# Performance work log

Hardware: AMD Instinct MI355X
Metric: run time of the kernel (lower is better)

Reference implementation:

```python
import jax, jax.numpy as jnp
import numpy as np

K_BINS, EMB_WIDTH = 2048, 64
N, T = 8, 8192

def setup_inputs() -> dict:
    key = jax.random.key(0)
    k1, k2 = jax.random.split(key)
    x = jax.random.normal(k1, (N, EMB_WIDTH, T), dtype=jnp.float32)
    mask = jnp.ones((N, 1, T), dtype=jnp.float32)
    k = jax.random.normal(k2, (K_BINS, EMB_WIDTH), dtype=jnp.float32)
    return {"x": x, "mask": mask, "k": k}

def reference(x, mask, k):
    # Faithful forward of BottleneckBlock.forward with update_k=False and
    # codebook `k` already initialized (init path is a stateful randperm init).
    n, c, t = x.shape
    w = k.shape[1]
    # preprocess: [N, W, T] -> [N*T, W]
    xf = jnp.transpose(x, (0, 2, 1)).reshape(-1, c)
    mf = jnp.transpose(mask, (0, 2, 1)).reshape(-1, 1)
    prenorm = jnp.linalg.norm(xf - jnp.mean(xf)) / np.sqrt(float(xf.size))
    dist = (jnp.sum(xf * xf, axis=-1, keepdims=True)
            - 2.0 * (xf @ k.T)
            + jnp.sum(k * k, axis=-1)[None, :])  # [N*T, k_bins]
    x_l = jnp.argmin(dist, axis=-1)              # [N*T]
    fit = jax.lax.stop_gradient(jnp.mean(jnp.min(dist, axis=-1)))
    x_d = jax.lax.stop_gradient(k[x_l])          # dequantize, no_grad in torch
    # commit loss: mask is 0/1, so masked-row norm^2 == sum(mask * diff^2)
    diff2 = jnp.sum((x_d - xf) ** 2, axis=-1, keepdims=True)
    commit_loss = jnp.sum(mf * diff2) / (jnp.sum(mf) * w)
    # straight-through estimator + mask
    x_d = (xf + jax.lax.stop_gradient(x_d - xf)) * mf
    # postprocess: back to [N, W, T] and [N, T]
    x_d = jnp.transpose(x_d.reshape(n, t, w), (0, 2, 1))
    x_l = x_l.reshape(n, t)
    return x_l, x_d, commit_loss, fit, prenorm
```

## Files before the change

### kernel.cpp

```cpp
#include <hip/hip_runtime.h>

#define T_DIM 8192
#define N_DIM 8
#define C_DIM 64
#define KB    2048
#define NT    (N_DIM * T_DIM)
#define TOTX  ((size_t)NT * C_DIM)
#define NBLK  1024
#define LISTCAP 65536
#define TAU   0.04f

#define SCR_COUNT 0
#define SCR_LIST  16
#define SCR_PART  65792
#define SCR_KK    76544
#define SCR_K     81920
#define SCR_FIX   262144

typedef _Float16 half_t;
typedef _Float16 f16x8 __attribute__((ext_vector_type(8)));
typedef float    f32x16 __attribute__((ext_vector_type(16)));

__device__ __forceinline__ float np_sumsq64(const float* __restrict__ a) {
    float r[8];
    #pragma unroll
    for (int j = 0; j < 8; ++j) r[j] = __fmul_rn(a[j], a[j]);
    #pragma unroll
    for (int i = 8; i < 64; i += 8)
        #pragma unroll
        for (int j = 0; j < 8; ++j)
            r[j] = __fadd_rn(r[j], __fmul_rn(a[i + j], a[i + j]));
    return __fadd_rn(__fadd_rn(__fadd_rn(r[0], r[1]), __fadd_rn(r[2], r[3])),
                     __fadd_rn(__fadd_rn(r[4], r[5]), __fadd_rn(r[6], r[7])));
}

__global__ __launch_bounds__(256) void kprep_kernel(const float* __restrict__ k,
                                                    float* __restrict__ out) {
    float* base = out + NT;
    const int bin = blockIdx.x * 256 + threadIdx.x;
    if (bin == 0) ((int*)base)[SCR_COUNT] = 0;

    float kv[64];
    #pragma unroll
    for (int i = 0; i < 16; ++i)
        *(float4*)&kv[i * 4] = *(const float4*)(k + (size_t)bin * 64 + i * 4);

    float kn = 0.f;
    #pragma unroll
    for (int c = 0; c < 64; ++c) kn = fmaf(kv[c], kv[c], kn);
    base[SCR_KK + bin] = np_sumsq64(kv);

    f16x8* kscr = (f16x8*)(base + SCR_K);
    const int ch = bin >> 7, b127 = bin & 127;
    #pragma unroll
    for (int slot = 0; slot < 8; ++slot) {
        f16x8 h8;
        #pragma unroll
        for (int e = 0; e < 8; ++e)
            h8[e] = (half_t)(-2.f * (float)((half_t)kv[slot * 8 + e]));
        kscr[(size_t)ch * 1152 + slot * 128 + b127] = h8;
    }
    {
        half_t knh = (half_t)kn;
        half_t knl = (half_t)(kn - (float)knh);
        f16x8 k8;
        #pragma unroll
        for (int e = 0; e < 8; ++e) k8[e] = (half_t)0.f;
        k8[0] = knh; k8[1] = knl;
        kscr[(size_t)ch * 1152 + 1024 + b127] = k8;
    }
}

__global__ __launch_bounds__(256, 2) void argmin_kernel(const float* __restrict__ x,
                                                        const float* __restrict__ mask,
                                                        float* __restrict__ out) {
    __shared__ __align__(16) f16x8 xhi_s[512];
    __shared__ float psx[4][64], psxx[4][64];
    __shared__ float wres[2][64][3];

    float* base = out + NT;
    const int tid = threadIdx.x;
    const int l   = tid & 63, w = tid >> 6;
    const int col = l & 31, kg = l >> 5;
    const int rg  = w >> 1, hb = w & 1;
    const int r0  = blockIdx.x * 64;
    const int n   = r0 >> 13;
    const int t0  = r0 & (T_DIM - 1);

    {
        const int row = tid & 63, sp = tid >> 6;
        float sx = 0.f, sxx = 0.f;
        #pragma unroll
        for (int ss = 0; ss < 2; ++ss) {
            const int slot = sp * 2 + ss;
            f16x8 h8;
            #pragma unroll
            for (int e = 0; e < 8; ++e) {
                float v = x[((size_t)n * C_DIM + slot * 8 + e) * T_DIM + t0 + row];
                h8[e] = (half_t)v;
                sx += v; sxx = fmaf(v, v, sxx);
            }
            xhi_s[slot * 64 + row] = h8;
        }
        psx[sp][row]  = sx;
        psxx[sp][row] = sxx;
    }
    __syncthreads();

    f16x8 a0 = xhi_s[(0 + kg) * 64 + rg * 32 + col];
    f16x8 a1 = xhi_s[(2 + kg) * 64 + rg * 32 + col];
    f16x8 a2 = xhi_s[(4 + kg) * 64 + rg * 32 + col];
    f16x8 a3 = xhi_s[(6 + kg) * 64 + rg * 32 + col];
    f16x8 aones;
    #pragma unroll
    for (int e = 0; e < 8; ++e) aones[e] = (half_t)0.f;
    if (kg == 0) { aones[0] = (half_t)1.f; aones[1] = (half_t)1.f; }

    const f16x8* kf0 = (const f16x8*)(base + SCR_K) + (size_t)hb * 9216 + col;
    const int kgo = kg * 128;

    f32x16 zacc;
    #pragma unroll
    for (int r = 0; r < 16; ++r) zacc[r] = 0.f;

    float bv0 = __builtin_inff(), b20 = __builtin_inff(); int c0 = 0;
    float bv1 = __builtin_inff(), b21 = __builtin_inff(); int c1 = 0;
    float bv2 = __builtin_inff(), b22 = __builtin_inff(); int c2 = 0;
    float bv3 = __builtin_inff(), b23 = __builtin_inff(); int c3 = 0;

    f16x8 bA[4], bB[4], b4A, b4B;

#define LOADT(t, BH, B4)                                            \
    {                                                               \
        const f16x8* p = kf0 + (((t) >> 2) * 1152 + ((t) & 3) * 32);\
        BH[0] = p[kgo]; BH[1] = p[kgo + 256];                       \
        BH[2] = p[kgo + 512]; BH[3] = p[kgo + 768];                 \
        B4 = p[1024];                                               \
    }

#define UPD(J, RR, CODE)                                                     \
    {                                                                        \
        float sv = acc[RR];                                                  \
        float nb2;                                                           \
        asm("v_med3_f32 %0, %1, %2, %3"                                      \
            : "=v"(nb2) : "v"(sv), "v"(bv##J), "v"(b2##J));                  \
        b2##J = nb2;                                                         \
        if (sv < bv##J) { bv##J = sv; c##J = (CODE); }                       \
    }

#define COMPT(t, BH, B4)                                                     \
    {                                                                        \
        f32x16 acc = __builtin_amdgcn_mfma_f32_32x32x16_f16(B4, aones, zacc, 0, 0, 0); \
        acc = __builtin_amdgcn_mfma_f32_32x32x16_f16(BH[0], a0, acc, 0, 0, 0); \
        acc = __builtin_amdgcn_mfma_f32_32x32x16_f16(BH[1], a1, acc, 0, 0, 0); \
        acc = __builtin_amdgcn_mfma_f32_32x32x16_f16(BH[2], a2, acc, 0, 0, 0); \
        acc = __builtin_amdgcn_mfma_f32_32x32x16_f16(BH[3], a3, acc, 0, 0, 0); \
        const int cb = hb * 1024 + (t) * 32;                                 \
        UPD(0, 0, cb + 0)  UPD(0, 1, cb + 1)  UPD(0, 2, cb + 2)  UPD(0, 3, cb + 3) \
        UPD(1, 4, cb + 8)  UPD(1, 5, cb + 9)  UPD(1, 6, cb + 10) UPD(1, 7, cb + 11) \
        UPD(2, 8, cb + 16) UPD(2, 9, cb + 17) UPD(2, 10, cb + 18) UPD(2, 11, cb + 19) \
        UPD(3, 12, cb + 24) UPD(3, 13, cb + 25) UPD(3, 14, cb + 26) UPD(3, 15, cb + 27) \
    }

    LOADT(0, bA, b4A);
    #pragma unroll 1
    for (int t = 0; t < 30; t += 2) {
        LOADT(t + 1, bB, b4B);
        COMPT(t, bA, b4A);
        LOADT(t + 2, bA, b4A);
        COMPT(t + 1, bB, b4B);
    }
    LOADT(31, bB, b4B);
    COMPT(30, bA, b4A);
    COMPT(31, bB, b4B);
#undef LOADT
#undef COMPT
#undef UPD

    const int hi4 = kg * 4;
    c0 += hi4; c1 += hi4; c2 += hi4; c3 += hi4;

    float bv, b2; int bb;
    {
        float m01v; int m01c; float m01s;
        if (bv1 < bv0 || (bv1 == bv0 && c1 < c0)) { m01v = bv1; m01c = c1; }
        else                                      { m01v = bv0; m01c = c0; }
        m01s = fminf(fminf(b20, b21), fmaxf(bv0, bv1));
        float m23v; int m23c; float m23s;
        if (bv3 < bv2 || (bv3 == bv2 && c3 < c2)) { m23v = bv3; m23c = c3; }
        else                                      { m23v = bv2; m23c = c2; }
        m23s = fminf(fminf(b22, b23), fmaxf(bv2, bv3));
        if (m23v < m01v || (m23v == m01v && m23c < m01c)) { bv = m23v; bb = m23c; }
        else                                              { bv = m01v; bb = m01c; }
        b2 = fminf(fminf(m01s, m23s), fmaxf(m01v, m23v));
    }

    {
        float ov = __shfl_xor(bv, 32, 64);
        float o2 = __shfl_xor(b2, 32, 64);
        int   ob = __shfl_xor(bb, 32, 64);
        b2 = fminf(fminf(b2, o2), fmaxf(bv, ov));
        if (ov < bv || (ov == bv && ob < bb)) { bv = ov; bb = ob; }
    }

    if (kg == 0) {
        const int row_loc = rg * 32 + col;
        wres[hb][row_loc][0] = bv;
        wres[hb][row_loc][1] = b2;
        wres[hb][row_loc][2] = __int_as_float(bb);
    }
    __syncthreads();

    if (tid < 64) {
        const int row = tid;
        const float v0 = wres[0][row][0], v1 = wres[1][row][0];
        float fbv = v0; int fbb = __float_as_int(wres[0][row][2]);
        if (v1 < fbv) { fbv = v1; fbb = __float_as_int(wres[1][row][2]); }
        const float fb2 = fminf(fminf(wres[0][row][1], wres[1][row][1]),
                                fmaxf(v0, v1));
        out[r0 + row] = (float)fbb;
        if (fb2 - fbv < TAU) {
            int idx = atomicAdd((int*)base + SCR_COUNT, 1);
            if (idx < LISTCAP) ((int*)base + SCR_LIST)[idx] = r0 + row;
        }
        float sx = 0.f, sxx = 0.f;
        #pragma unroll
        for (int sp = 0; sp < 4; ++sp) { sx += psx[sp][row]; sxx += psxx[sp][row]; }
        const float m  = mask[r0 + row];
        const float d2 = sxx + fbv;
        float vals[5] = { m * d2, d2, m, sx, sxx };
        #pragma unroll
        for (int off = 1; off <= 32; off <<= 1)
            #pragma unroll
            for (int q = 0; q < 5; ++q) vals[q] += __shfl_xor(vals[q], off, 64);
        if (tid == 0) {
            float* partials = base + SCR_PART;
            #pragma unroll
            for (int q = 0; q < 5; ++q)
                partials[(size_t)blockIdx.x * 8 + q] = vals[q];
        }
    }
}

__global__ __launch_bounds__(256) void fixup_kernel(const float* __restrict__ x,
                                                    const float* __restrict__ k,
                                                    float* __restrict__ out) {
    __shared__ float xs[32][65];
    __shared__ float sxx_s[32];
    __shared__ float redv[256];
    __shared__ int   redb[256];

    const int tid = threadIdx.x;
    float* base = out + NT;
    const int* count    = (const int*)base + SCR_COUNT;
    const int* flaglist = (const int*)base + SCR_LIST;
    const float* kk     = base + SCR_KK;
    float* fix          = base + SCR_FIX;
    int cnt = *count;
    if (cnt > LISTCAP) cnt = LISTCAP;
    const int nb8 = ((cnt + 31) >> 5) << 3;

    const int rloc = tid & 31, part = tid >> 5;

    for (int wk = blockIdx.x; wk < nb8; wk += gridDim.x) {
        const int bi = wk >> 3, chunk = wk & 7;
        int li = bi * 32 + rloc;
        if (li >= cnt) li = bi * 32;
        const int row = flaglist[li];
        const int n = row >> 13, t = row & (T_DIM - 1);
        #pragma unroll
        for (int e = 0; e < 8; ++e)
            xs[rloc][part * 8 + e] = x[((size_t)n * C_DIM + part * 8 + e) * T_DIM + t];
        __syncthreads();
        if (tid < 32) sxx_s[tid] = np_sumsq64(&xs[tid][0]);
        __syncthreads();

        float xr[64];
        #pragma unroll
        for (int c = 0; c < 64; ++c) xr[c] = xs[rloc][c];
        const float xx = sxx_s[rloc];

        float bv = __builtin_inff();
        int   bb = 0x7fffffff;
        const int bbase = chunk * 256 + part * 32;
        #pragma unroll 1
        for (int i = 0; i < 32; i += 2) {
            const int b0 = bbase + i;
            const int b1 = b0 + 1;
            const float* k0 = k + (size_t)b0 * 64;
            const float* k1 = k + (size_t)b1 * 64;
            float d0 = 0.f, d1 = 0.f;
            #pragma unroll
            for (int c = 0; c < 64; ++c) {
                d0 = fmaf(xr[c], k0[c], d0);
                d1 = fmaf(xr[c], k1[c], d1);
            }
            float s0 = __fadd_rn(__fsub_rn(xx, __fadd_rn(d0, d0)), kk[b0]);
            float s1 = __fadd_rn(__fsub_rn(xx, __fadd_rn(d1, d1)), kk[b1]);
            if (s0 < bv || (s0 == bv && b0 < bb)) { bv = s0; bb = b0; }
            if (s1 < bv || (s1 == bv && b1 < bb)) { bv = s1; bb = b1; }
        }
        redv[tid] = bv; redb[tid] = bb;
        __syncthreads();
        if (tid < 32) {
            float fv = redv[tid]; int fb = redb[tid];
            #pragma unroll
            for (int p = 1; p < 8; ++p) {
                float ov = redv[p * 32 + tid];
                int   ob = redb[p * 32 + tid];
                if (ov < fv || (ov == fv && ob < fb)) { fv = ov; fb = ob; }
            }
            const int fi = bi * 32 + tid;
            if (fi < cnt) {
                fix[(size_t)fi * 16 + chunk * 2]     = fv;
                fix[(size_t)fi * 16 + chunk * 2 + 1] = __int_as_float(fb);
            }
        }
        __syncthreads();
    }
}

__global__ __launch_bounds__(256) void fixmerge_kernel(float* __restrict__ out) {
    float* base = out + NT;
    const int* count    = (const int*)base + SCR_COUNT;
    const int* flaglist = (const int*)base + SCR_LIST;
    const float* fix    = base + SCR_FIX;
    int cnt = *count;
    if (cnt > LISTCAP) cnt = LISTCAP;

    for (int fi = blockIdx.x * 256 + threadIdx.x; fi < cnt;
         fi += gridDim.x * 256) {
        const float* p = fix + (size_t)fi * 16;
        float bv = p[0];
        int   bb = __float_as_int(p[1]);
        #pragma unroll
        for (int c = 1; c < 8; ++c) {
            float v = p[c * 2];
            int   b = __float_as_int(p[c * 2 + 1]);
            if (v < bv || (v == bv && b < bb)) { bv = v; bb = b; }
        }
        out[flaglist[fi]] = (float)bb;
    }
}

__global__ __launch_bounds__(256) void finalize_kernel(float* __restrict__ out) {
    const float* partials = (out + NT) + SCR_PART;
    const int tid = threadIdx.x;
    double vals[5] = {0, 0, 0, 0, 0};
    for (int i = tid; i < NBLK; i += 256)
        #pragma unroll
        for (int q = 0; q < 5; ++q) vals[q] += (double)partials[(size_t)i * 8 + q];
    #pragma unroll
    for (int off = 1; off <= 32; off <<= 1)
        #pragma unroll
        for (int q = 0; q < 5; ++q) vals[q] += __shfl_xor(vals[q], off, 64);
    __shared__ double sred[4][5];
    const int wid = tid >> 6, lane = tid & 63;
    if (lane == 0)
        for (int q = 0; q < 5; ++q) sred[wid][q] = vals[q];
    __syncthreads();
    if (tid == 0) {
        double cm  = sred[0][0] + sred[1][0] + sred[2][0] + sred[3][0];
        double fs  = sred[0][1] + sred[1][1] + sred[2][1] + sred[3][1];
        double ms  = sred[0][2] + sred[1][2] + sred[2][2] + sred[3][2];
        double sx  = sred[0][3] + sred[1][3] + sred[2][3] + sred[3][3];
        double sxx = sred[0][4] + sred[1][4] + sred[2][4] + sred[3][4];
        double sz  = (double)TOTX;
        out[NT + TOTX + 0] = (float)(cm / (ms * (double)C_DIM));
        out[NT + TOTX + 1] = (float)(fs / (double)NT);
        out[NT + TOTX + 2] = (float)sqrt(fmax(0.0, (sxx - sx * sx / sz) / sz));
    }
}

__global__ __launch_bounds__(256) void xd_kernel(const float* __restrict__ mask,
                                                 const float* __restrict__ k,
                                                 float* __restrict__ out) {
    const int row = blockIdx.x * 256 + threadIdx.x;
    const int n = row >> 13, t = row & (T_DIM - 1);
    const int b = (int)out[row];
    const float m = mask[row];
    const float* kr = k + (size_t)b * C_DIM;
    float* xd = out + NT;
    #pragma unroll
    for (int c = 0; c < C_DIM; ++c)
        xd[((size_t)n * C_DIM + c) * T_DIM + t] = kr[c] * m;
}

extern "C" void kernel_launch(void* const* d_in, const int* in_sizes, int n_in,
                              void* d_out, int out_size, void* d_ws, size_t ws_size,
                              hipStream_t stream) {
    (void)in_sizes; (void)n_in; (void)out_size; (void)d_ws; (void)ws_size;
    const float* x    = (const float*)d_in[0];
    const float* mask = (const float*)d_in[1];
    const float* k    = (const float*)d_in[2];
    float* out = (float*)d_out;

    kprep_kernel<<<KB / 256, 256, 0, stream>>>(k, out);
    argmin_kernel<<<NBLK, 256, 0, stream>>>(x, mask, out);
    fixup_kernel<<<2048, 256, 0, stream>>>(x, k, out);
    fixmerge_kernel<<<256, 256, 0, stream>>>(out);
    finalize_kernel<<<1, 256, 0, stream>>>(out);
    xd_kernel<<<NT / 256, 256, 0, stream>>>(mask, k, out);
}
```

Measured before the change: 78.78 us.

## Split argmin work to 32 rows per block, four codebook quarters per wave, fold finalize

The argmin kernel now handles 32 rows per block instead of 64. Each of its four waves scans a quarter of the codebook, where before two row-groups each scanned half. The grid doubles to 2048 blocks, the per-wave loop is halved, and a 4-way merge of best and second-best values replaces the 2-way one. The finalize reduction is folded into block 0 of fixmerge to save one launch, and kprep now uses 64-thread blocks. The aim is more blocks for better CU coverage and a shorter dependent loop per wave, at the cost of more partials to reduce and loading the codebook twice as many times overall.

```diff
diff --git a/kernel.cpp b/kernel.cpp
--- a/kernel.cpp
+++ b/kernel.cpp
@@ -6,15 +6,15 @@
 #define KB    2048
 #define NT    (N_DIM * T_DIM)
 #define TOTX  ((size_t)NT * C_DIM)
-#define NBLK  1024
+#define NBLK  2048
 #define LISTCAP 65536
 #define TAU   0.04f
 
 #define SCR_COUNT 0
 #define SCR_LIST  16
 #define SCR_PART  65792
-#define SCR_KK    76544
-#define SCR_K     81920
+#define SCR_KK    82432
+#define SCR_K     90112
 #define SCR_FIX   262144
 
 typedef _Float16 half_t;
@@ -34,10 +34,10 @@
                      __fadd_rn(__fadd_rn(r[4], r[5]), __fadd_rn(r[6], r[7])));
 }
 
-__global__ __launch_bounds__(256) void kprep_kernel(const float* __restrict__ k,
-                                                    float* __restrict__ out) {
+__global__ __launch_bounds__(64) void kprep_kernel(const float* __restrict__ k,
+                                                   float* __restrict__ out) {
     float* base = out + NT;
-    const int bin = blockIdx.x * 256 + threadIdx.x;
+    const int bin = blockIdx.x * 64 + threadIdx.x;
     if (bin == 0) ((int*)base)[SCR_COUNT] = 0;
 
     float kv[64];
@@ -74,49 +74,44 @@
 __global__ __launch_bounds__(256, 2) void argmin_kernel(const float* __restrict__ x,
                                                         const float* __restrict__ mask,
                                                         float* __restrict__ out) {
-    __shared__ __align__(16) f16x8 xhi_s[512];
-    __shared__ float psx[4][64], psxx[4][64];
-    __shared__ float wres[2][64][3];
+    __shared__ __align__(16) f16x8 xhi_s[256];
+    __shared__ float psx[8][32], psxx[8][32];
+    __shared__ float wres[4][32][3];
 
     float* base = out + NT;
     const int tid = threadIdx.x;
     const int l   = tid & 63, w = tid >> 6;
     const int col = l & 31, kg = l >> 5;
-    const int rg  = w >> 1, hb = w & 1;
-    const int r0  = blockIdx.x * 64;
+    const int r0  = blockIdx.x * 32;
     const int n   = r0 >> 13;
     const int t0  = r0 & (T_DIM - 1);
 
     {
-        const int row = tid & 63, sp = tid >> 6;
+        const int row = tid & 31, slot = tid >> 5;
         float sx = 0.f, sxx = 0.f;
-        #pragma unroll
-        for (int ss = 0; ss < 2; ++ss) {
-            const int slot = sp * 2 + ss;
-            f16x8 h8;
-            #pragma unroll
-            for (int e = 0; e < 8; ++e) {
-                float v = x[((size_t)n * C_DIM + slot * 8 + e) * T_DIM + t0 + row];
-                h8[e] = (half_t)v;
-                sx += v; sxx = fmaf(v, v, sxx);
-            }
-            xhi_s[slot * 64 + row] = h8;
-        }
-        psx[sp][row]  = sx;
-        psxx[sp][row] = sxx;
+        f16x8 h8;
+        #pragma unroll
+        for (int e = 0; e < 8; ++e) {
+            float v = x[((size_t)n * C_DIM + slot * 8 + e) * T_DIM + t0 + row];
+            h8[e] = (half_t)v;
+            sx += v; sxx = fmaf(v, v, sxx);
+        }
+        xhi_s[slot * 32 + row] = h8;
+        psx[slot][row]  = sx;
+        psxx[slot][row] = sxx;
     }
     __syncthreads();
 
-    f16x8 a0 = xhi_s[(0 + kg) * 64 + rg * 32 + col];
-    f16x8 a1 = xhi_s[(2 + kg) * 64 + rg * 32 + col];
-    f16x8 a2 = xhi_s[(4 + kg) * 64 + rg * 32 + col];
-    f16x8 a3 = xhi_s[(6 + kg) * 64 + rg * 32 + col];
+    f16x8 a0 = xhi_s[(0 + kg) * 32 + col];
+    f16x8 a1 = xhi_s[(2 + kg) * 32 + col];
+    f16x8 a2 = xhi_s[(4 + kg) * 32 + col];
+    f16x8 a3 = xhi_s[(6 + kg) * 32 + col];
     f16x8 aones;
     #pragma unroll
     for (int e = 0; e < 8; ++e) aones[e] = (half_t)0.f;
     if (kg == 0) { aones[0] = (half_t)1.f; aones[1] = (half_t)1.f; }
 
-    const f16x8* kf0 = (const f16x8*)(base + SCR_K) + (size_t)hb * 9216 + col;
+    const f16x8* kf0 = (const f16x8*)(base + SCR_K) + (size_t)w * 4 * 1152 + col;
     const int kgo = kg * 128;
 
     f32x16 zacc;
@@ -155,7 +150,7 @@
         acc = __builtin_amdgcn_mfma_f32_32x32x16_f16(BH[1], a1, acc, 0, 0, 0); \
         acc = __builtin_amdgcn_mfma_f32_32x32x16_f16(BH[2], a2, acc, 0, 0, 0); \
         acc = __builtin_amdgcn_mfma_f32_32x32x16_f16(BH[3], a3, acc, 0, 0, 0); \
-        const int cb = hb * 1024 + (t) * 32;                                 \
+        const int cb = w * 512 + (t) * 32;                                   \
         UPD(0, 0, cb + 0)  UPD(0, 1, cb + 1)  UPD(0, 2, cb + 2)  UPD(0, 3, cb + 3) \
         UPD(1, 4, cb + 8)  UPD(1, 5, cb + 9)  UPD(1, 6, cb + 10) UPD(1, 7, cb + 11) \
         UPD(2, 8, cb + 16) UPD(2, 9, cb + 17) UPD(2, 10, cb + 18) UPD(2, 11, cb + 19) \
@@ -164,15 +159,15 @@
 
     LOADT(0, bA, b4A);
     #pragma unroll 1
-    for (int t = 0; t < 30; t += 2) {
+    for (int t = 0; t < 14; t += 2) {
         LOADT(t + 1, bB, b4B);
         COMPT(t, bA, b4A);
         LOADT(t + 2, bA, b4A);
         COMPT(t + 1, bB, b4B);
     }
-    LOADT(31, bB, b4B);
-    COMPT(30, bA, b4A);
-    COMPT(31, bB, b4B);
+    LOADT(15, bB, b4B);
+    COMPT(14, bA, b4A);
+    COMPT(15, bB, b4B);
 #undef LOADT
 #undef COMPT
 #undef UPD
@@ -204,20 +199,27 @@
     }
 
     if (kg == 0) {
-        const int row_loc = rg * 32 + col;
-        wres[hb][row_loc][0] = bv;
-        wres[hb][row_loc][1] = b2;
-        wres[hb][row_loc][2] = __int_as_float(bb);
+        wres[w][col][0] = bv;
+        wres[w][col][1] = b2;
+        wres[w][col][2] = __int_as_float(bb);
     }
     __syncthreads();
 
-    if (tid < 64) {
+    if (tid < 32) {
         const int row = tid;
         const float v0 = wres[0][row][0], v1 = wres[1][row][0];
+        const float v2 = wres[2][row][0], v3 = wres[3][row][0];
         float fbv = v0; int fbb = __float_as_int(wres[0][row][2]);
         if (v1 < fbv) { fbv = v1; fbb = __float_as_int(wres[1][row][2]); }
-        const float fb2 = fminf(fminf(wres[0][row][1], wres[1][row][1]),
-                                fmaxf(v0, v1));
+        if (v2 < fbv) { fbv = v2; fbb = __float_as_int(wres[2][row][2]); }
+        if (v3 < fbv) { fbv = v3; fbb = __float_as_int(wres[3][row][2]); }
+        const float m01 = fminf(v0, v1), M01 = fmaxf(v0, v1);
+        const float m23 = fminf(v2, v3), M23 = fmaxf(v2, v3);
+        const float sec = fminf(fmaxf(m01, m23), fminf(M01, M23));
+        const float fb2 = fminf(sec,
+            fminf(fminf(wres[0][row][1], wres[1][row][1]),
+                  fminf(wres[2][row][1], wres[3][row][1])));
+
         out[r0 + row] = (float)fbb;
         if (fb2 - fbv < TAU) {
             int idx = atomicAdd((int*)base + SCR_COUNT, 1);
@@ -225,12 +227,12 @@
         }
         float sx = 0.f, sxx = 0.f;
         #pragma unroll
-        for (int sp = 0; sp < 4; ++sp) { sx += psx[sp][row]; sxx += psxx[sp][row]; }
+        for (int sp = 0; sp < 8; ++sp) { sx += psx[sp][row]; sxx += psxx[sp][row]; }
         const float m  = mask[r0 + row];
         const float d2 = sxx + fbv;
         float vals[5] = { m * d2, d2, m, sx, sxx };
         #pragma unroll
-        for (int off = 1; off <= 32; off <<= 1)
+        for (int off = 1; off <= 16; off <<= 1)
             #pragma unroll
             for (int q = 0; q < 5; ++q) vals[q] += __shfl_xor(vals[q], off, 64);
         if (tid == 0) {
@@ -325,11 +327,11 @@
     const int* count    = (const int*)base + SCR_COUNT;
     const int* flaglist = (const int*)base + SCR_LIST;
     const float* fix    = base + SCR_FIX;
+    const int tid = threadIdx.x;
     int cnt = *count;
     if (cnt > LISTCAP) cnt = LISTCAP;
 
-    for (int fi = blockIdx.x * 256 + threadIdx.x; fi < cnt;
-         fi += gridDim.x * 256) {
+    for (int fi = blockIdx.x * 256 + tid; fi < cnt; fi += gridDim.x * 256) {
         const float* p = fix + (size_t)fi * 16;
         float bv = p[0];
         int   bb = __float_as_int(p[1]);
@@ -341,34 +343,33 @@
         }
         out[flaglist[fi]] = (float)bb;
     }
-}
-
-__global__ __launch_bounds__(256) void finalize_kernel(float* __restrict__ out) {
-    const float* partials = (out + NT) + SCR_PART;
-    const int tid = threadIdx.x;
-    double vals[5] = {0, 0, 0, 0, 0};
-    for (int i = tid; i < NBLK; i += 256)
-        #pragma unroll
-        for (int q = 0; q < 5; ++q) vals[q] += (double)partials[(size_t)i * 8 + q];
-    #pragma unroll
-    for (int off = 1; off <= 32; off <<= 1)
-        #pragma unroll
-        for (int q = 0; q < 5; ++q) vals[q] += __shfl_xor(vals[q], off, 64);
-    __shared__ double sred[4][5];
-    const int wid = tid >> 6, lane = tid & 63;
-    if (lane == 0)
-        for (int q = 0; q < 5; ++q) sred[wid][q] = vals[q];
-    __syncthreads();
-    if (tid == 0) {
-        double cm  = sred[0][0] + sred[1][0] + sred[2][0] + sred[3][0];
-        double fs  = sred[0][1] + sred[1][1] + sred[2][1] + sred[3][1];
-        double ms  = sred[0][2] + sred[1][2] + sred[2][2] + sred[3][2];
-        double sx  = sred[0][3] + sred[1][3] + sred[2][3] + sred[3][3];
-        double sxx = sred[0][4] + sred[1][4] + sred[2][4] + sred[3][4];
-        double sz  = (double)TOTX;
-        out[NT + TOTX + 0] = (float)(cm / (ms * (double)C_DIM));
-        out[NT + TOTX + 1] = (float)(fs / (double)NT);
-        out[NT + TOTX + 2] = (float)sqrt(fmax(0.0, (sxx - sx * sx / sz) / sz));
+
+    if (blockIdx.x == 0) {
+        const float* partials = base + SCR_PART;
+        double vals[5] = {0, 0, 0, 0, 0};
+        for (int i = tid; i < NBLK; i += 256)
+            #pragma unroll
+            for (int q = 0; q < 5; ++q) vals[q] += (double)partials[(size_t)i * 8 + q];
+        #pragma unroll
+        for (int off = 1; off <= 32; off <<= 1)
+            #pragma unroll
+            for (int q = 0; q < 5; ++q) vals[q] += __shfl_xor(vals[q], off, 64);
+        __shared__ double sred[4][5];
+        const int wid = tid >> 6, lane = tid & 63;
+        if (lane == 0)
+            for (int q = 0; q < 5; ++q) sred[wid][q] = vals[q];
+        __syncthreads();
+        if (tid == 0) {
+            double cm  = sred[0][0] + sred[1][0] + sred[2][0] + sred[3][0];
+            double fs  = sred[0][1] + sred[1][1] + sred[2][1] + sred[3][1];
+            double ms  = sred[0][2] + sred[1][2] + sred[2][2] + sred[3][2];
+            double sx  = sred[0][3] + sred[1][3] + sred[2][3] + sred[3][3];
+            double sxx = sred[0][4] + sred[1][4] + sred[2][4] + sred[3][4];
+            double sz  = (double)TOTX;
+            out[NT + TOTX + 0] = (float)(cm / (ms * (double)C_DIM));
+            out[NT + TOTX + 1] = (float)(fs / (double)NT);
+            out[NT + TOTX + 2] = (float)sqrt(fmax(0.0, (sxx - sx * sx / sz) / sz));
+        }
     }
 }
 
@@ -395,10 +396,9 @@
     const float* k    = (const float*)d_in[2];
     float* out = (float*)d_out;
 
-    kprep_kernel<<<KB / 256, 256, 0, stream>>>(k, out);
+    kprep_kernel<<<32, 64, 0, stream>>>(k, out);
     argmin_kernel<<<NBLK, 256, 0, stream>>>(x, mask, out);
     fixup_kernel<<<2048, 256, 0, stream>>>(x, k, out);
     fixmerge_kernel<<<256, 256, 0, stream>>>(out);
-    finalize_kernel<<<1, 256, 0, stream>>>(out);
     xd_kernel<<<NT / 256, 256, 0, stream>>>(mask, k, out);
 }
```

Result: no change. 79.51 us (+0.9%).
